# Performance work log

Hardware: AMD Instinct MI355X
Metric: run time of the kernel (lower is better)

Reference implementation:

```python
import jax, jax.numpy as jnp
import numpy as np

N = 50000        # nodes
E = 800000       # edges (avg degree 16)
F_IN = 128
H = 128
C = 16


def setup_inputs() -> dict:
    key = jax.random.key(0)
    ks = jax.random.split(key, 12)
    x = jax.random.normal(ks[0], (N, F_IN), dtype=jnp.float32)
    edges = jax.random.randint(ks[1], (2, E), 0, N, dtype=jnp.int32)
    dims = [(F_IN, H), (H, H // 2), (H // 2, H // 4), (H // 4, H // 8), (H // 8, C)]
    params = {}
    for i, (di, do) in enumerate(dims):
        params[f"W{i+1}"] = jax.random.normal(ks[2 + 2 * i], (di, do), dtype=jnp.float32) * (1.0 / np.sqrt(di)).astype(np.float32)
        params[f"b{i+1}"] = jax.random.normal(ks[3 + 2 * i], (do,), dtype=jnp.float32) * 0.01
    return {"x": x, "edges": edges, **params}


def reference(x, edges, W1, b1, W2, b2, W3, b3, W4, b4, W5, b5):
    src, dst = edges[0], edges[1]
    ones = jnp.ones((E,), x.dtype)
    # symmetric ('both') normalization with degree clamped to >= 1 (DGL GraphConv default)
    out_deg = jnp.clip(jax.ops.segment_sum(ones, src, num_segments=N), 1.0, None)
    in_deg = jnp.clip(jax.ops.segment_sum(ones, dst, num_segments=N), 1.0, None)
    norm_src = (out_deg ** -0.5)[:, None]   # [N,1]
    norm_dst = (in_deg ** -0.5)[:, None]    # [N,1]

    def graph_conv(h, W, b):
        h = h @ W                                  # dense transform first (out <= in)
        msgs = (h * norm_src)[src]                 # [E, d_out] gather
        agg = jax.ops.segment_sum(msgs, dst, num_segments=N)  # scatter-add SpMM
        return agg * norm_dst + b

    h = x
    for W, b in ((W1, b1), (W2, b2), (W3, b3), (W4, b4), (W5, b5)):
        h = jax.nn.relu(graph_conv(h, W, b))
    return h
```

## Files before the change

kernel.cpp:

```cpp
#include <hip/hip_runtime.h>
#include <hip/hip_bf16.h>


#define THREADS 256
#define HIST_B 128
#define HWORDS 12500
#define RS_BLOCKS 196
#define G1BLKS 1564
#define C4 (HIST_B / 4)

typedef __attribute__((ext_vector_type(8))) short short8_t;
typedef __attribute__((ext_vector_type(4))) float float4_t;

__device__ __forceinline__ unsigned short f2bf_rne(float f) {
    unsigned u = __builtin_bit_cast(unsigned, f);
    unsigned r = u + 0x7fffu + ((u >> 16) & 1u);
    return (unsigned short)(r >> 16);
}
__device__ __forceinline__ float bf2f(unsigned short h) {
    return __builtin_bit_cast(float, ((unsigned)h) << 16);
}

template<int NT, bool NORM, bool ASCALE>
__device__ __forceinline__ void quant_epilogue(float4_t* acc, const float* __restrict__ norm,
                                               const float* __restrict__ ascale,
                                               short* __restrict__ outq, float* __restrict__ qscale,
                                               int M, int blk, int tid,
                                               int ostride, int ocol0, int qstride, int qoff) {
    const int w    = tid >> 6;
    const int lane = tid & 63;
    const int ln   = lane & 15;
    const int quad = lane >> 4;
    const int orow = blk * 64 + w * 16 + quad * 4;
#pragma unroll
    for (int i = 0; i < 4; ++i) {
        int r = orow + i;
        float m = 0.f;
#pragma unroll
        for (int nt = 0; nt < NT; ++nt) m = fmaxf(m, fabsf(acc[nt][i]));
#pragma unroll
        for (int off = 1; off < 16; off <<= 1) m = fmaxf(m, __shfl_xor(m, off));
        float s = 1.f;
        if (NORM) s = (r < M) ? norm[r] : 0.f;
        if (ASCALE && r < M) s *= ascale[r];
        float rowmax = m * s;
        float inv = (rowmax > 0.f) ? (32767.f / rowmax) : 0.f;
        if (r < M) {
            if (ln == 0) qscale[r * qstride + qoff] = rowmax * (1.f / 32767.f);
#pragma unroll
            for (int nt = 0; nt < NT; ++nt)
                outq[(size_t)r * ostride + ocol0 + nt * 16 + ln] =
                    (short)(int)__builtin_rintf(acc[nt][i] * s * inv);
        }
    }
}

template<int K, int NOUT, bool NORM>
__device__ __forceinline__ void gemm_core(const float* __restrict__ A,
                                          const short* lh, const short* ll,
                                          const float* __restrict__ norm,
                                          short* __restrict__ outq, float* __restrict__ qscale,
                                          int M, int blk, int tid,
                                          int ostride, int ocol0, int qstride, int qoff) {
    constexpr int Kp  = (K + 31) & ~31;
    constexpr int STR = Kp + 8;
    constexpr int NT  = NOUT / 16;
    const int w    = tid >> 6;
    const int lane = tid & 63;
    const int ln   = lane & 15;
    const int quad = lane >> 4;
    const int row  = blk * 64 + w * 16 + ln;
    const bool rv  = row < M;

    float4_t acc[NT];
#pragma unroll
    for (int i = 0; i < NT; ++i) acc[i] = (float4_t){0.f, 0.f, 0.f, 0.f};

#pragma unroll
    for (int kt = 0; kt < Kp / 32; ++kt) {
        const int k0 = kt * 32 + quad * 8;
        float a[8];
        if (rv && k0 < K) {
            float4 v0 = *(const float4*)&A[(size_t)row * K + k0];
            float4 v1 = *(const float4*)&A[(size_t)row * K + k0 + 4];
            a[0] = v0.x; a[1] = v0.y; a[2] = v0.z; a[3] = v0.w;
            a[4] = v1.x; a[5] = v1.y; a[6] = v1.z; a[7] = v1.w;
        } else {
#pragma unroll
            for (int j = 0; j < 8; ++j) a[j] = 0.f;
        }
        short8_t ahi, alo;
#pragma unroll
        for (int j = 0; j < 8; ++j) {
            unsigned short h = f2bf_rne(a[j]);
            ahi[j] = (short)h;
            alo[j] = (short)f2bf_rne(a[j] - bf2f(h));
        }
#pragma unroll
        for (int nt = 0; nt < NT; ++nt) {
            const int bidx = (nt * 16 + ln) * STR + kt * 32 + quad * 8;
            short8_t bh = *(const short8_t*)&lh[bidx];
            short8_t bl = *(const short8_t*)&ll[bidx];
            acc[nt] = __builtin_amdgcn_mfma_f32_16x16x32_bf16(ahi, bh, acc[nt], 0, 0, 0);
            acc[nt] = __builtin_amdgcn_mfma_f32_16x16x32_bf16(ahi, bl, acc[nt], 0, 0, 0);
            acc[nt] = __builtin_amdgcn_mfma_f32_16x16x32_bf16(alo, bh, acc[nt], 0, 0, 0);
        }
    }
    quant_epilogue<NT, NORM, false>(acc, norm, nullptr, outq, qscale, M, blk, tid,
                                    ostride, ocol0, qstride, qoff);
}

template<int K, int NOUT>
__device__ __forceinline__ void gemm_core_q(const short* __restrict__ Aq,
                                            const float* __restrict__ ascale,
                                            const short* lh, const short* ll,
                                            const float* __restrict__ norm,
                                            short* __restrict__ outq, float* __restrict__ qscale,
                                            int M, int blk, int tid) {
    constexpr int Kp  = (K + 31) & ~31;
    constexpr int STR = Kp + 8;
    constexpr int NT  = NOUT / 16;
    const int w    = tid >> 6;
    const int lane = tid & 63;
    const int ln   = lane & 15;
    const int quad = lane >> 4;
    const int row  = blk * 64 + w * 16 + ln;
    const bool rv  = row < M;

    float4_t acc[NT];
#pragma unroll
    for (int i = 0; i < NT; ++i) acc[i] = (float4_t){0.f, 0.f, 0.f, 0.f};

#pragma unroll
    for (int kt = 0; kt < Kp / 32; ++kt) {
        const int k0 = kt * 32 + quad * 8;
        short8_t qv = (short8_t)(short)0;
        if (rv && k0 < K) qv = *(const short8_t*)&Aq[(size_t)row * K + k0];
        short8_t ahi, alo;
#pragma unroll
        for (int j = 0; j < 8; ++j) {
            float a = (float)qv[j];
            unsigned short h = f2bf_rne(a);
            ahi[j] = (short)h;
            alo[j] = (short)f2bf_rne(a - bf2f(h));
        }
#pragma unroll
        for (int nt = 0; nt < NT; ++nt) {
            const int bidx = (nt * 16 + ln) * STR + kt * 32 + quad * 8;
            short8_t bh = *(const short8_t*)&lh[bidx];
            short8_t bl = *(const short8_t*)&ll[bidx];
            acc[nt] = __builtin_amdgcn_mfma_f32_16x16x32_bf16(ahi, bh, acc[nt], 0, 0, 0);
            acc[nt] = __builtin_amdgcn_mfma_f32_16x16x32_bf16(ahi, bl, acc[nt], 0, 0, 0);
            acc[nt] = __builtin_amdgcn_mfma_f32_16x16x32_bf16(alo, bh, acc[nt], 0, 0, 0);
        }
    }
    quant_epilogue<NT, true, true>(acc, norm, ascale, outq, qscale, M, blk, tid,
                                   NOUT, 0, 1, 0);
}

template<int K, int NOUT, int DINP>
__device__ __forceinline__ void gemm_core_lds(const float* As,
                                              const short* lh, const short* ll,
                                              const float* __restrict__ norm,
                                              short* __restrict__ outq, float* __restrict__ qscale,
                                              int M, int blk, int tid) {
    constexpr int Kp  = (K + 31) & ~31;
    constexpr int STR = Kp + 8;
    constexpr int NT  = NOUT / 16;
    const int w    = tid >> 6;
    const int lane = tid & 63;
    const int ln   = lane & 15;
    const int quad = lane >> 4;
    const int rloc = w * 16 + ln;
    const bool rv  = (blk * 64 + rloc) < M;

    float4_t acc[NT];
#pragma unroll
    for (int i = 0; i < NT; ++i) acc[i] = (float4_t){0.f, 0.f, 0.f, 0.f};

#pragma unroll
    for (int kt = 0; kt < Kp / 32; ++kt) {
        const int k0 = kt * 32 + quad * 8;
        float a[8];
        if (rv && k0 < K) {
            float4 v0 = *(const float4*)&As[rloc * DINP + k0];
            float4 v1 = *(const float4*)&As[rloc * DINP + k0 + 4];
            a[0] = v0.x; a[1] = v0.y; a[2] = v0.z; a[3] = v0.w;
            a[4] = v1.x; a[5] = v1.y; a[6] = v1.z; a[7] = v1.w;
        } else {
#pragma unroll
            for (int j = 0; j < 8; ++j) a[j] = 0.f;
        }
        short8_t ahi, alo;
#pragma unroll
        for (int j = 0; j < 8; ++j) {
            unsigned short h = f2bf_rne(a[j]);
            ahi[j] = (short)h;
            alo[j] = (short)f2bf_rne(a[j] - bf2f(h));
        }
#pragma unroll
        for (int nt = 0; nt < NT; ++nt) {
            const int bidx = (nt * 16 + ln) * STR + kt * 32 + quad * 8;
            short8_t bh = *(const short8_t*)&lh[bidx];
            short8_t bl = *(const short8_t*)&ll[bidx];
            acc[nt] = __builtin_amdgcn_mfma_f32_16x16x32_bf16(ahi, bh, acc[nt], 0, 0, 0);
            acc[nt] = __builtin_amdgcn_mfma_f32_16x16x32_bf16(ahi, bl, acc[nt], 0, 0, 0);
            acc[nt] = __builtin_amdgcn_mfma_f32_16x16x32_bf16(alo, bh, acc[nt], 0, 0, 0);
        }
    }
    quant_epilogue<NT, true, false>(acc, norm, nullptr, outq, qscale, M, blk, tid,
                                    NOUT, 0, 1, 0);
}

__device__ __forceinline__ void conv_one(const float* __restrict__ W, short* __restrict__ hi,
                                         short* __restrict__ lo, int K, int NOUT, int STR, int i) {
    int n = i / STR;
    int kk = i % STR;
    float v = (kk < K) ? W[(size_t)kk * NOUT + n] : 0.f;
    unsigned short h = f2bf_rne(v);
    hi[i] = (short)h;
    lo[i] = (short)f2bf_rne(v - bf2f(h));
}

__global__ __launch_bounds__(THREADS)
void packed0_kernel(const float* __restrict__ x, const float* __restrict__ W1,
                    const float* __restrict__ W2, const float* __restrict__ W3,
                    const float* __restrict__ W4, const float* __restrict__ W5,
                    short* __restrict__ tq, float* __restrict__ qscale2,
                    const int* __restrict__ src, const int* __restrict__ dst,
                    unsigned* __restrict__ p_src, unsigned* __restrict__ p_dst,
                    unsigned char* __restrict__ rank, int* __restrict__ flags,
                    short* w2h, short* w2l, short* w3h, short* w3l,
                    short* w4h, short* w4l, short* w5h, short* w5l,
                    int E, int chunk, int N) {
    __shared__ __align__(16) char smem[50048];
    const int blk = blockIdx.x;
    const int t = threadIdx.x;

    if (blk < G1BLKS) {
        const int h  = blk & 1;
        const int gb = blk >> 1;
        short* lh = (short*)smem;
        short* ll = (short*)smem + 8704;
        for (int j = t; j < 128 * 64; j += THREADS) {
            int kk = j >> 6, n = j & 63;
            float v = W1[kk * 128 + h * 64 + n];
            unsigned short hh = f2bf_rne(v);
            lh[n * 136 + kk] = (short)hh;
            ll[n * 136 + kk] = (short)f2bf_rne(v - bf2f(hh));
        }
        __syncthreads();
        gemm_core<128, 64, false>(x, lh, ll, nullptr, tq, qscale2, N, gb, t,
                                  128, h * 64, 2, h);
    } else if (blk < G1BLKS + 2 * HIST_B) {
        unsigned* bins = (unsigned*)smem;
        const int hb = blk - G1BLKS;
        const bool is_dst = hb < HIST_B;
        const int b = is_dst ? hb : hb - HIST_B;
        const int e0 = b * chunk;
        int e1 = e0 + chunk; if (e1 > E) e1 = E;
        const int* __restrict__ idx = is_dst ? dst : src;
        unsigned* __restrict__ pout = is_dst ? p_dst : p_src;

        for (int w = t; w < HWORDS; w += THREADS) bins[w] = 0;
        __syncthreads();
        for (int e = e0 + t; e < e1; e += THREADS) {
            int d = idx[e];
            unsigned sh = (unsigned)(d & 3) * 8u;
            unsigned old = atomicAdd(&bins[d >> 2], 1u << sh);
            if (is_dst) rank[e] = (unsigned char)((old >> sh) & 0xffu);
        }
        __syncthreads();
        for (int w = t; w < HWORDS; w += THREADS)
            pout[(size_t)b * HWORDS + w] = bins[w];
    } else {
        int cb = blk - G1BLKS - 2 * HIST_B;
        if (cb == 48) {
            flags[t] = 0;
            return;
        }
        int i = cb * THREADS + t;
        if (i < 8704)                        conv_one(W2, w2h, w2l, 128, 64, 136, i);
        else if ((i -= 8704) < 2304)         conv_one(W3, w3h, w3l, 64, 32, 72, i);
        else if ((i -= 2304) < 640)          conv_one(W4, w4h, w4l, 32, 16, 40, i);
        else { i -= 640;                     conv_one(W5, w5h, w5l, 16, 16, 40, i); }
    }
}

__global__ __launch_bounds__(THREADS)
void reduce_scan_kernel(const unsigned* __restrict__ p_src, unsigned* __restrict__ p_dst,
                        float* __restrict__ norm_src, float* __restrict__ norm_dst,
                        float* __restrict__ qscale2, int* __restrict__ row_ptr,
                        int* __restrict__ flags, int N) {
    __shared__ unsigned qd[4][64];
    __shared__ unsigned qs[4][64];
    __shared__ int sscan[64];
    __shared__ int bexcl_sh;
    const int t  = threadIdx.x;
    const int b  = blockIdx.x;
    const int q  = t >> 6;
    const int wl = t & 63;
    const int w  = b * 64 + wl;
    const bool wv = (w < HWORDS);

    unsigned vals[C4];
    unsigned dsum = 0, ssum = 0;
    if (wv) {
#pragma unroll
        for (int i = 0; i < C4; ++i) {
            int c = q * C4 + i;
            vals[i] = p_dst[(size_t)c * HWORDS + w];
            dsum += vals[i];
        }
#pragma unroll
        for (int i = 0; i < C4; ++i) {
            int c = q * C4 + i;
            ssum += p_src[(size_t)c * HWORDS + w];
        }
    }
    qd[q][wl] = dsum;
    qs[q][wl] = ssum;
    __syncthreads();

    unsigned off = 0, dfull = 0, sfull = 0;
#pragma unroll
    for (int qq = 0; qq < 4; ++qq) {
        unsigned v = qd[qq][wl];
        if (qq < q) off += v;
        dfull += v;
        sfull += qs[qq][wl];
    }

    if (wv) {
        unsigned run = off;
#pragma unroll
        for (int i = 0; i < C4; ++i) {
            int c = q * C4 + i;
            p_dst[(size_t)c * HWORDS + w] = run;
            run += vals[i];
        }
    }

    int d0 = 0, d1 = 0, d2 = 0, d3 = 0, wdeg = 0;
    if (q == 0) {
        d0 = (int)(dfull & 0xffu); d1 = (int)((dfull >> 8) & 0xffu);
        d2 = (int)((dfull >> 16) & 0xffu); d3 = (int)(dfull >> 24);
        wdeg = d0 + d1 + d2 + d3;
        if (wv) {
#pragma unroll
            for (int l = 0; l < 4; ++l) {
                int node = 4 * w + l;
                int dd = (l == 0) ? d0 : (l == 1) ? d1 : (l == 2) ? d2 : d3;
                int ds = (int)((sfull >> (8 * l)) & 0xffu);
                norm_dst[node] = rsqrtf((float)(dd < 1 ? 1 : dd));
                float ns = rsqrtf((float)(ds < 1 ? 1 : ds));
                norm_src[node] = ns;
                qscale2[2 * node]     *= ns;
                qscale2[2 * node + 1] *= ns;
            }
        }
        sscan[wl] = wv ? wdeg : 0;
    }
    __syncthreads();
    for (int o = 1; o < 64; o <<= 1) {
        int u = 0;
        if (t < 64 && t >= o) u = sscan[t - o];
        __syncthreads();
        if (t < 64) sscan[t] += u;
        __syncthreads();
    }
    const int btotal = sscan[63];

    if (t == 0) atomicExch(&flags[b], btotal + 1);
    if (t < 64) {
        int v = 0;
        for (int p = t; p < b; p += 64) {
            int f;
            do { f = atomicAdd(&flags[p], 0); } while (f == 0);
            v += f - 1;
        }
#pragma unroll
        for (int o = 1; o < 64; o <<= 1) v += __shfl_xor(v, o);
        if (t == 0) bexcl_sh = v;
    }
    __syncthreads();

    if (q == 0 && wv) {
        int pre = bexcl_sh + sscan[wl] - wdeg;
        int n0 = 4 * w;
        row_ptr[n0 + 0] = pre; pre += d0;
        row_ptr[n0 + 1] = pre; pre += d1;
        row_ptr[n0 + 2] = pre; pre += d2;
        row_ptr[n0 + 3] = pre;
    }
    if (b == RS_BLOCKS - 1 && t == 0) row_ptr[N] = bexcl_sh + btotal;
}

__global__ __launch_bounds__(THREADS)
void scatter_kernel(const int* __restrict__ src, const int* __restrict__ dst,
                    const unsigned char* __restrict__ rank,
                    const int* __restrict__ row_ptr, const unsigned* __restrict__ p_dst,
                    int* __restrict__ col, int E, int chunk) {
    const int bc  = blockIdx.x >> 2;
    const int sub = blockIdx.x & 3;
    const int qch = (chunk + 3) >> 2;
    const int e0 = bc * chunk;
    int e1 = e0 + chunk; if (e1 > E) e1 = E;
    int s = e0 + sub * qch;
    int send = s + qch; if (send > e1) send = e1;
    for (int e = s + threadIdx.x; e < send; e += THREADS) {
        int d = dst[e];
        unsigned sh = (unsigned)(d & 3) * 8u;
        unsigned pre = (p_dst[(size_t)bc * HWORDS + (d >> 2)] >> sh) & 0xffu;
        col[row_ptr[d] + (int)pre + (int)rank[e]] = src[e];
    }
}

__global__ __launch_bounds__(THREADS)
void agg1_q_kernel(const short* __restrict__ tq, const float* __restrict__ qscale2,
                   const int* __restrict__ row_ptr, const int* __restrict__ col,
                   const float* __restrict__ norm_dst, const float* __restrict__ bias,
                   short* __restrict__ outq, float* __restrict__ qs_out, int N) {
    const int tid  = threadIdx.x;
    const int ln   = tid & 15;
    const int ep   = (tid >> 4) & 1;
    const int g    = tid >> 5;
    const int node = blockIdx.x * 8 + g;
    if (node >= N) return;

    const int half = ln >> 3;
    const int beg = row_ptr[node];
    const int end = row_ptr[node + 1];

    float acc[8];
#pragma unroll
    for (int c = 0; c < 8; ++c) acc[c] = 0.f;

    int j = beg + ep;
    for (; j + 2 < end; j += 4) {
        int s0 = col[j];
        int s1 = col[j + 2];
        short8_t v0 = *(const short8_t*)&tq[(size_t)s0 * 128 + ln * 8];
        short8_t v1 = *(const short8_t*)&tq[(size_t)s1 * 128 + ln * 8];
        float c0 = qscale2[2 * s0 + half];
        float c1 = qscale2[2 * s1 + half];
#pragma unroll
        for (int c = 0; c < 8; ++c)
            acc[c] += (float)v0[c] * c0 + (float)v1[c] * c1;
    }
    if (j < end) {
        int s0 = col[j];
        short8_t v0 = *(const short8_t*)&tq[(size_t)s0 * 128 + ln * 8];
        float c0 = qscale2[2 * s0 + half];
#pragma unroll
        for (int c = 0; c < 8; ++c) acc[c] += (float)v0[c] * c0;
    }

#pragma unroll
    for (int c = 0; c < 8; ++c) acc[c] += __shfl_xor(acc[c], 16);

    float nd = norm_dst[node];
    float vals[8];
    float m = 0.f;
#pragma unroll
    for (int c = 0; c < 8; ++c) {
        vals[c] = fmaxf(acc[c] * nd + bias[ln * 8 + c], 0.f);
        m = fmaxf(m, vals[c]);
    }
#pragma unroll
    for (int off = 1; off < 16; off <<= 1) m = fmaxf(m, __shfl_xor(m, off));
    float inv = (m > 0.f) ? (32767.f / m) : 0.f;

    if (ep == 0) {
        short8_t q;
#pragma unroll
        for (int c = 0; c < 8; ++c) q[c] = (short)(int)__builtin_rintf(vals[c] * inv);
        *(short8_t*)&outq[(size_t)node * 128 + ln * 8] = q;
        if (ln == 0) qs_out[node] = m * (1.f / 32767.f);
    }
}

template<int K, int NOUT>
__global__ __launch_bounds__(THREADS)
void gemm_mfma_q_kernel(const short* __restrict__ Aq, const float* __restrict__ ascale,
                        const short* __restrict__ wt_hi, const short* __restrict__ wt_lo,
                        const float* __restrict__ norm,
                        short* __restrict__ outq, float* __restrict__ qscale, int M) {
    constexpr int Kp  = (K + 31) & ~31;
    constexpr int STR = Kp + 8;

    __shared__ short lh[NOUT * STR];
    __shared__ short ll[NOUT * STR];

    const int tid = threadIdx.x;
    {
        constexpr int CNT = NOUT * STR / 2;
        const int* gh = (const int*)wt_hi;
        const int* gl = (const int*)wt_lo;
        int* sh = (int*)lh;
        int* sl = (int*)ll;
        for (int i = tid; i < CNT; i += THREADS) { sh[i] = gh[i]; sl[i] = gl[i]; }
    }
    __syncthreads();
    gemm_core_q<K, NOUT>(Aq, ascale, lh, ll, norm, outq, qscale, M, blockIdx.x, tid);
}

template<int D>
__global__ __launch_bounds__(THREADS)
void agg_q_kernel(const short* __restrict__ tq, const float* __restrict__ qscale,
                  const int* __restrict__ row_ptr, const int* __restrict__ col,
                  const float* __restrict__ norm_dst, const float* __restrict__ bias,
                  float* __restrict__ out, int N) {
    constexpr int TPN = D / 8;
    constexpr int NPB = THREADS / TPN;
    const int tid  = threadIdx.x;
    const int ln   = tid % TPN;
    const int g    = tid / TPN;
    const int node = blockIdx.x * NPB + g;
    if (node >= N) return;

    const int beg = row_ptr[node];
    const int end = row_ptr[node + 1];

    float acc[8];
#pragma unroll
    for (int c = 0; c < 8; ++c) acc[c] = 0.f;

    int j = beg;
    for (; j + 3 < end; j += 4) {
        int s0 = col[j], s1 = col[j + 1], s2 = col[j + 2], s3 = col[j + 3];
        short8_t v0 = *(const short8_t*)&tq[(size_t)s0 * D + ln * 8];
        short8_t v1 = *(const short8_t*)&tq[(size_t)s1 * D + ln * 8];
        short8_t v2 = *(const short8_t*)&tq[(size_t)s2 * D + ln * 8];
        short8_t v3 = *(const short8_t*)&tq[(size_t)s3 * D + ln * 8];
        float c0 = qscale[s0], c1 = qscale[s1], c2 = qscale[s2], c3 = qscale[s3];
#pragma unroll
        for (int c = 0; c < 8; ++c)
            acc[c] += (float)v0[c] * c0 + (float)v1[c] * c1
                    + (float)v2[c] * c2 + (float)v3[c] * c3;
    }
    for (; j < end; ++j) {
        int s0 = col[j];
        short8_t v0 = *(const short8_t*)&tq[(size_t)s0 * D + ln * 8];
        float c0 = qscale[s0];
#pragma unroll
        for (int c = 0; c < 8; ++c) acc[c] += (float)v0[c] * c0;
    }

    float nd = norm_dst[node];
    float4 b0 = *(const float4*)&bias[ln * 8];
    float4 b1 = *(const float4*)&bias[ln * 8 + 4];
    float4 o0, o1;
    o0.x = fmaxf(acc[0] * nd + b0.x, 0.f);
    o0.y = fmaxf(acc[1] * nd + b0.y, 0.f);
    o0.z = fmaxf(acc[2] * nd + b0.z, 0.f);
    o0.w = fmaxf(acc[3] * nd + b0.w, 0.f);
    o1.x = fmaxf(acc[4] * nd + b1.x, 0.f);
    o1.y = fmaxf(acc[5] * nd + b1.y, 0.f);
    o1.z = fmaxf(acc[6] * nd + b1.z, 0.f);
    o1.w = fmaxf(acc[7] * nd + b1.w, 0.f);
    *(float4*)&out[(size_t)node * D + ln * 8] = o0;
    *(float4*)&out[(size_t)node * D + ln * 8 + 4] = o1;
}

template<int DIN, int NOUT>
__global__ __launch_bounds__(THREADS)
void fused_agg_gemm_kernel(const short* __restrict__ tq_in, const float* __restrict__ qs_in,
                           const int* __restrict__ row_ptr, const int* __restrict__ col,
                           const float* __restrict__ norm_dst, const float* __restrict__ bias,
                           const short* __restrict__ wt_hi, const short* __restrict__ wt_lo,
                           const float* __restrict__ norm_src,
                           short* __restrict__ tq_out, float* __restrict__ qs_out, int N) {
    constexpr int Kp   = (DIN + 31) & ~31;
    constexpr int STR  = Kp + 8;
    constexpr int DINP = DIN + 4;
    constexpr int TPN  = DIN / 8;

    __shared__ float As[64 * DINP];
    __shared__ short lh[NOUT * STR];
    __shared__ short ll[NOUT * STR];

    const int tid = threadIdx.x;
    {
        constexpr int CNT = NOUT * STR / 2;
        const int* gh = (const int*)wt_hi;
        const int* gl = (const int*)wt_lo;
        int* sh = (int*)lh;
        int* sl = (int*)ll;
        for (int i = tid; i < CNT; i += THREADS) { sh[i] = gh[i]; sl[i] = gl[i]; }
    }

    const int ln = tid % TPN;
    for (int n0 = tid / TPN; n0 < 64; n0 += THREADS / TPN) {
        const int node = blockIdx.x * 64 + n0;
        if (node < N) {
            const int beg = row_ptr[node];
            const int end = row_ptr[node + 1];
            float acc[8];
#pragma unroll
            for (int c = 0; c < 8; ++c) acc[c] = 0.f;
            int j = beg;
            for (; j + 3 < end; j += 4) {
                int s0 = col[j], s1 = col[j + 1], s2 = col[j + 2], s3 = col[j + 3];
                short8_t v0 = *(const short8_t*)&tq_in[(size_t)s0 * DIN + ln * 8];
                short8_t v1 = *(const short8_t*)&tq_in[(size_t)s1 * DIN + ln * 8];
                short8_t v2 = *(const short8_t*)&tq_in[(size_t)s2 * DIN + ln * 8];
                short8_t v3 = *(const short8_t*)&tq_in[(size_t)s3 * DIN + ln * 8];
                float c0 = qs_in[s0], c1 = qs_in[s1], c2 = qs_in[s2], c3 = qs_in[s3];
#pragma unroll
                for (int c = 0; c < 8; ++c)
                    acc[c] += (float)v0[c] * c0 + (float)v1[c] * c1
                            + (float)v2[c] * c2 + (float)v3[c] * c3;
            }
            for (; j < end; ++j) {
                int s0 = col[j];
                short8_t v0 = *(const short8_t*)&tq_in[(size_t)s0 * DIN + ln * 8];
                float c0 = qs_in[s0];
#pragma unroll
                for (int c = 0; c < 8; ++c) acc[c] += (float)v0[c] * c0;
            }
            float nd = norm_dst[node];
#pragma unroll
            for (int c = 0; c < 8; ++c)
                As[n0 * DINP + ln * 8 + c] = fmaxf(acc[c] * nd + bias[ln * 8 + c], 0.f);
        }
    }
    __syncthreads();

    gemm_core_lds<DIN, NOUT, DINP>(As, lh, ll, norm_src, tq_out, qs_out, N, blockIdx.x, tid);
}

extern "C" void kernel_launch(void* const* d_in, const int* in_sizes, int n_in,
                              void* d_out, int out_size, void* d_ws, size_t ws_size,
                              hipStream_t stream) {
    const float* x     = (const float*)d_in[0];
    const int*   edges = (const int*)d_in[1];
    const float* W1 = (const float*)d_in[2];  const float* b1 = (const float*)d_in[3];
    const float* W2 = (const float*)d_in[4];  const float* b2 = (const float*)d_in[5];
    const float* W3 = (const float*)d_in[6];  const float* b3 = (const float*)d_in[7];
    const float* W4 = (const float*)d_in[8];  const float* b4 = (const float*)d_in[9];
    const float* W5 = (const float*)d_in[10]; const float* b5 = (const float*)d_in[11];

    const int N = in_sizes[0] / 128;
    const int E = in_sizes[1] / 2;
    const int* src = edges;
    const int* dst = edges + E;

    char* ws = (char*)d_ws;
    size_t off = 0;
    auto carve = [&](size_t bytes) -> void* {
        void* p = ws + off;
        off += (bytes + 255) & ~(size_t)255;
        return p;
    };
    short* tqA      = (short*)carve((size_t)N * 128 * 2);
    short* tqB      = (short*)carve((size_t)N * 64 * 2);
    short* tqH      = (short*)carve((size_t)N * 128 * 2);
    float* norm_src = (float*)carve((size_t)N * 4);
    float* norm_dst = (float*)carve((size_t)N * 4);
    int*   row_ptr  = (int*)carve((size_t)(N + 1) * 4);
    int*   col      = (int*)carve((size_t)E * 4);
    float* qsA      = (float*)carve((size_t)2 * N * 4);
    float* qsB      = (float*)carve((size_t)N * 4);
    float* qsH      = (float*)carve((size_t)N * 4);
    int*   flags    = (int*)carve((size_t)256 * 4);
    short* wts      = (short*)carve((size_t)24576 * 2);
    unsigned* p_src = (unsigned*)carve((size_t)HIST_B * HWORDS * 4);
    unsigned* p_dst = (unsigned*)carve((size_t)HIST_B * HWORDS * 4);
    unsigned char* rank = (unsigned char*)carve((size_t)E);
    (void)ws_size;

    short* w2h = wts;            short* w2l = w2h + 8704;
    short* w3h = w2l + 8704;     short* w3l = w3h + 2304;
    short* w4h = w3l + 2304;     short* w4l = w4h + 640;
    short* w5h = w4l + 640;      short* w5l = w5h + 640;

    const int chunk = (E + HIST_B - 1) / HIST_B;
    const int gridG = (N + 63) / 64;

    packed0_kernel<<<G1BLKS + 2 * HIST_B + 49, THREADS, 0, stream>>>(
        x, W1, W2, W3, W4, W5, tqA, qsA, src, dst, p_src, p_dst, rank, flags,
        w2h, w2l, w3h, w3l, w4h, w4l, w5h, w5l, E, chunk, N);

    reduce_scan_kernel<<<RS_BLOCKS, THREADS, 0, stream>>>(
        p_src, p_dst, norm_src, norm_dst, qsA, row_ptr, flags, N);

    scatter_kernel<<<4 * HIST_B, THREADS, 0, stream>>>(src, dst, rank, row_ptr, p_dst, col, E, chunk);

    agg1_q_kernel<<<(N + 7) / 8, THREADS, 0, stream>>>(
        tqA, qsA, row_ptr, col, norm_dst, b1, tqH, qsH, N);

    gemm_mfma_q_kernel<128, 64><<<gridG, THREADS, 0, stream>>>(
        tqH, qsH, w2h, w2l, norm_src, tqA, qsA, N);

    fused_agg_gemm_kernel<64, 32><<<gridG, THREADS, 0, stream>>>(
        tqA, qsA, row_ptr, col, norm_dst, b2, w3h, w3l, norm_src, tqB, qsB, N);
    fused_agg_gemm_kernel<32, 16><<<gridG, THREADS, 0, stream>>>(
        tqB, qsB, row_ptr, col, norm_dst, b3, w4h, w4l, norm_src, tqA, qsA, N);
    fused_agg_gemm_kernel<16, 16><<<gridG, THREADS, 0, stream>>>(
        tqA, qsA, row_ptr, col, norm_dst, b4, w5h, w5l, norm_src, tqB, qsB, N);

    agg_q_kernel<16><<<(N + 127) / 128, THREADS, 0, stream>>>(
        tqB, qsB, row_ptr, col, norm_dst, b5, (float*)d_out, N);
}
```

Before: 260.7 us.

## Process both W1 column halves per block, loading x rows once

The first-layer GEMM previously launched two blocks per 64-row tile, one per 64-column half of W1, so each row of x was read and split into bf16 hi/lo twice. Now one block loads and converts its x tile into registers once and loops over both W1 halves, re-staging W1 in shared memory between them. This halves x global traffic and conversion work and halves the GEMM block count. In exchange each block runs two serialized weight-staging and MFMA phases with extra barriers, and register pressure rises from holding the converted A fragments.

```diff
diff --git a/kernel.cpp b/kernel.cpp
--- a/kernel.cpp
+++ b/kernel.cpp
@@ -6,7 +6,7 @@
 #define HIST_B 128
 #define HWORDS 12500
 #define RS_BLOCKS 196
-#define G1BLKS 1564
+#define G1BLKS 782
 #define C4 (HIST_B / 4)
 
 typedef __attribute__((ext_vector_type(8))) short short8_t;
@@ -53,61 +53,6 @@
                     (short)(int)__builtin_rintf(acc[nt][i] * s * inv);
         }
     }
-}
-
-template<int K, int NOUT, bool NORM>
-__device__ __forceinline__ void gemm_core(const float* __restrict__ A,
-                                          const short* lh, const short* ll,
-                                          const float* __restrict__ norm,
-                                          short* __restrict__ outq, float* __restrict__ qscale,
-                                          int M, int blk, int tid,
-                                          int ostride, int ocol0, int qstride, int qoff) {
-    constexpr int Kp  = (K + 31) & ~31;
-    constexpr int STR = Kp + 8;
-    constexpr int NT  = NOUT / 16;
-    const int w    = tid >> 6;
-    const int lane = tid & 63;
-    const int ln   = lane & 15;
-    const int quad = lane >> 4;
-    const int row  = blk * 64 + w * 16 + ln;
-    const bool rv  = row < M;
-
-    float4_t acc[NT];
-#pragma unroll
-    for (int i = 0; i < NT; ++i) acc[i] = (float4_t){0.f, 0.f, 0.f, 0.f};
-
-#pragma unroll
-    for (int kt = 0; kt < Kp / 32; ++kt) {
-        const int k0 = kt * 32 + quad * 8;
-        float a[8];
-        if (rv && k0 < K) {
-            float4 v0 = *(const float4*)&A[(size_t)row * K + k0];
-            float4 v1 = *(const float4*)&A[(size_t)row * K + k0 + 4];
-            a[0] = v0.x; a[1] = v0.y; a[2] = v0.z; a[3] = v0.w;
-            a[4] = v1.x; a[5] = v1.y; a[6] = v1.z; a[7] = v1.w;
-        } else {
-#pragma unroll
-            for (int j = 0; j < 8; ++j) a[j] = 0.f;
-        }
-        short8_t ahi, alo;
-#pragma unroll
-        for (int j = 0; j < 8; ++j) {
-            unsigned short h = f2bf_rne(a[j]);
-            ahi[j] = (short)h;
-            alo[j] = (short)f2bf_rne(a[j] - bf2f(h));
-        }
-#pragma unroll
-        for (int nt = 0; nt < NT; ++nt) {
-            const int bidx = (nt * 16 + ln) * STR + kt * 32 + quad * 8;
-            short8_t bh = *(const short8_t*)&lh[bidx];
-            short8_t bl = *(const short8_t*)&ll[bidx];
-            acc[nt] = __builtin_amdgcn_mfma_f32_16x16x32_bf16(ahi, bh, acc[nt], 0, 0, 0);
-            acc[nt] = __builtin_amdgcn_mfma_f32_16x16x32_bf16(ahi, bl, acc[nt], 0, 0, 0);
-            acc[nt] = __builtin_amdgcn_mfma_f32_16x16x32_bf16(alo, bh, acc[nt], 0, 0, 0);
-        }
-    }
-    quant_epilogue<NT, NORM, false>(acc, norm, nullptr, outq, qscale, M, blk, tid,
-                                    ostride, ocol0, qstride, qoff);
 }
 
 template<int K, int NOUT>
@@ -238,20 +183,66 @@
     const int t = threadIdx.x;
 
     if (blk < G1BLKS) {
-        const int h  = blk & 1;
-        const int gb = blk >> 1;
         short* lh = (short*)smem;
         short* ll = (short*)smem + 8704;
-        for (int j = t; j < 128 * 64; j += THREADS) {
-            int kk = j >> 6, n = j & 63;
-            float v = W1[kk * 128 + h * 64 + n];
-            unsigned short hh = f2bf_rne(v);
-            lh[n * 136 + kk] = (short)hh;
-            ll[n * 136 + kk] = (short)f2bf_rne(v - bf2f(hh));
-        }
-        __syncthreads();
-        gemm_core<128, 64, false>(x, lh, ll, nullptr, tq, qscale2, N, gb, t,
-                                  128, h * 64, 2, h);
+
+        const int lane = t & 63;
+        const int ln   = lane & 15;
+        const int quad = lane >> 4;
+        const int row  = blk * 64 + (t >> 6) * 16 + ln;
+        const bool rv  = row < N;
+
+        short8_t ahi[4], alo[4];
+#pragma unroll
+        for (int kt = 0; kt < 4; ++kt) {
+            const int k0 = kt * 32 + quad * 8;
+            float a[8];
+            if (rv) {
+                float4 v0 = *(const float4*)&x[(size_t)row * 128 + k0];
+                float4 v1 = *(const float4*)&x[(size_t)row * 128 + k0 + 4];
+                a[0] = v0.x; a[1] = v0.y; a[2] = v0.z; a[3] = v0.w;
+                a[4] = v1.x; a[5] = v1.y; a[6] = v1.z; a[7] = v1.w;
+            } else {
+#pragma unroll
+                for (int j = 0; j < 8; ++j) a[j] = 0.f;
+            }
+#pragma unroll
+            for (int j = 0; j < 8; ++j) {
+                unsigned short h = f2bf_rne(a[j]);
+                ahi[kt][j] = (short)h;
+                alo[kt][j] = (short)f2bf_rne(a[j] - bf2f(h));
+            }
+        }
+
+        for (int h = 0; h < 2; ++h) {
+            for (int j = t; j < 128 * 64; j += THREADS) {
+                int kk = j >> 6, n = j & 63;
+                float v = W1[kk * 128 + h * 64 + n];
+                unsigned short hh = f2bf_rne(v);
+                lh[n * 136 + kk] = (short)hh;
+                ll[n * 136 + kk] = (short)f2bf_rne(v - bf2f(hh));
+            }
+            __syncthreads();
+
+            float4_t acc[4];
+#pragma unroll
+            for (int i = 0; i < 4; ++i) acc[i] = (float4_t){0.f, 0.f, 0.f, 0.f};
+#pragma unroll
+            for (int kt = 0; kt < 4; ++kt) {
+#pragma unroll
+                for (int nt = 0; nt < 4; ++nt) {
+                    const int bidx = (nt * 16 + ln) * 136 + kt * 32 + quad * 8;
+                    short8_t bh = *(const short8_t*)&lh[bidx];
+                    short8_t bl = *(const short8_t*)&ll[bidx];
+                    acc[nt] = __builtin_amdgcn_mfma_f32_16x16x32_bf16(ahi[kt], bh, acc[nt], 0, 0, 0);
+                    acc[nt] = __builtin_amdgcn_mfma_f32_16x16x32_bf16(ahi[kt], bl, acc[nt], 0, 0, 0);
+                    acc[nt] = __builtin_amdgcn_mfma_f32_16x16x32_bf16(alo[kt], bh, acc[nt], 0, 0, 0);
+                }
+            }
+            quant_epilogue<4, false, false>(acc, nullptr, nullptr, tq, qscale2, N, blk, t,
+                                            128, h * 64, 2, h);
+            if (h == 0) __syncthreads();
+        }
     } else if (blk < G1BLKS + 2 * HIST_B) {
         unsigned* bins = (unsigned*)smem;
         const int hb = blk - G1BLKS;
```

Measured after the change: 259.5 us. Within noise of the previous version (-0.5%).
